# Optimization experiments

Measured on AMD Instinct MI355X. Metric: run time of the kernel, lower is better.

Reference implementation:

```python
import jax, jax.numpy as jnp
import numpy as np

BS, NS, NSTEP = 128, 1024, 8
IN_DIM, HID, MLP = 768, 512, 512
NEG = -100000.0


def setup_inputs() -> dict:
    key = jax.random.key(0)
    ks = jax.random.split(key, 12)
    s_h = 1.0 / np.sqrt(HID)
    s_cat = 1.0 / np.sqrt(HID + IN_DIM)
    s_m = 1.0 / np.sqrt(MLP)
    # gumbel noise implements Categorical sampling as argmax(logits + gumbel)
    u = jax.random.uniform(ks[9], (NSTEP, BS, NS), jnp.float32, 1e-7, 1.0 - 1e-7)
    return {
        "target_emb": jax.random.normal(ks[0], (BS, IN_DIM), jnp.float32),
        "ctx_emb": jax.random.normal(ks[1], (BS, NS, IN_DIM), jnp.float32),
        "target_len": jax.random.randint(ks[2], (BS,), 1, 32),
        "ctx_len": jax.random.randint(ks[3], (BS,), NSTEP, NS + 1),
        "n_step": NSTEP,
        "W_ih": jax.random.normal(ks[4], (4 * HID, IN_DIM), jnp.float32) * s_h,
        "W_hh": jax.random.normal(ks[5], (4 * HID, HID), jnp.float32) * s_h,
        "b_ih": jnp.zeros((4 * HID,), jnp.float32),
        "b_hh": jnp.zeros((4 * HID,), jnp.float32),
        "W1c": jax.random.normal(ks[6], (MLP, IN_DIM), jnp.float32) * s_cat,
        "W1h": jax.random.normal(ks[7], (MLP, HID), jnp.float32) * s_cat,
        "b1": jnp.zeros((MLP,), jnp.float32),
        "w2": jax.random.normal(ks[8], (MLP,), jnp.float32) * s_m,
        "b2": jnp.zeros((), jnp.float32),
        "gumbel": -jnp.log(-jnp.log(u)),
    }


def reference(target_emb, ctx_emb, target_len, ctx_len, n_step,
              W_ih, W_hh, b_ih, b_hh, W1c, W1h, b1, w2, b2, gumbel):
    bs, ns, in_dim = ctx_emb.shape
    hid = W_hh.shape[1]
    # mlp1 split: ctx part is constant across steps (concat([ctx, h]) @ W1^T = ctx@W1c^T + h@W1h^T)
    ctx_part = jnp.einsum('bnd,md->bnm', ctx_emb, W1c) + b1  # [bs, ns, mlp]
    mask0 = jnp.where(jnp.arange(ns)[None, :] >= ctx_len[:, None], NEG, 0.0).astype(jnp.float32)
    h0 = jnp.zeros((bs, hid), jnp.float32)
    c0 = jnp.zeros((bs, hid), jnp.float32)
    lp0 = jnp.zeros((bs,), jnp.float32)
    batch_idx = jnp.arange(bs)

    def step(carry, g):
        h, c, mask, x, lp = carry
        # LSTMCell (torch gate order: i, f, g, o); dropout is identity (eval semantics)
        gates = x @ W_ih.T + b_ih + h @ W_hh.T + b_hh
        i_g, f_g, g_g, o_g = jnp.split(gates, 4, axis=-1)
        c_new = jax.nn.sigmoid(f_g) * c + jax.nn.sigmoid(i_g) * jnp.tanh(g_g)
        h_new = jax.nn.sigmoid(o_g) * jnp.tanh(c_new)
        # attention-style MLP score
        pre = ctx_part + (h_new @ W1h.T)[:, None, :]          # [bs, ns, mlp]
        sc = jnp.tanh(pre) @ w2 + b2 + mask                   # [bs, ns]
        # Categorical(probs=softmax(sc)).sample() via Gumbel-argmax
        out = jnp.argmax(sc + g, axis=-1)                     # [bs]
        lp = lp + jnp.take_along_axis(jax.nn.log_softmax(sc, axis=-1), out[:, None], 1)[:, 0]
        mask = mask.at[batch_idx, out].set(NEG)
        x_new = jnp.take_along_axis(ctx_emb, out[:, None, None], axis=1)[:, 0, :]
        return (h_new, c_new, mask, x_new, lp), out

    (h, c, mask, x, log_probs), outputs = jax.lax.scan(
        step, (h0, c0, mask0, target_emb, lp0), gumbel)
    return outputs, log_probs
```

## Files before the change

kernel.cpp:

```cpp
#include <hip/hip_runtime.h>
#include <hip/hip_bf16.h>

#define BSZ 128
#define NSQ 1024
#define NSTEPC 8
#define IND 768
#define HIDD 512
#define G4D 2048
#define MLPD 512
#define KXD 1280
#define NEGV -100000.0f
#define KSG 16
#define KSH 8
#define MSPLIT 4

typedef __attribute__((ext_vector_type(4))) float f32x4;
typedef __attribute__((ext_vector_type(8))) short short8v;

__device__ __forceinline__ void split2(float4 f0, float4 f1, short8v& hi, short8v& lo) {
  float fv[8] = {f0.x, f0.y, f0.z, f0.w, f1.x, f1.y, f1.z, f1.w};
#pragma unroll
  for (int j = 0; j < 8; ++j) {
    const unsigned ub = __builtin_bit_cast(unsigned, fv[j]);
    const unsigned hb = ub & 0xFFFF0000u;
    const float lf = fv[j] - __builtin_bit_cast(float, hb);
    hi[j] = (short)(hb >> 16);
    lo[j] = (short)(__builtin_bit_cast(unsigned, lf) >> 16);
  }
}

__device__ __forceinline__ float tanh_fast(float x) {
  x = fminf(fmaxf(x, -15.0f), 15.0f);
  float e = __builtin_amdgcn_exp2f(x * 2.8853900817779268f);
  float r = __builtin_amdgcn_rcpf(e + 1.0f);
  return fmaf(-2.0f, r, 1.0f);
}

__global__ __launch_bounds__(256) void k_prep_wfrag(
    const float* __restrict__ W1c,
    unsigned short* __restrict__ wfh, unsigned short* __restrict__ wfl) {
  const int c = blockIdx.x * 256 + threadIdx.x;
  if (c >= 49152) return;
  const int row = c / 96, wc = c - row * 96;
  const int w = row >> 6;
  const int f = (row >> 4) & 3, l15 = row & 15;
  const int t = wc >> 2, l4 = wc & 3;
  const size_t unit = (((size_t)(w * 24 + t) * 4 + f) * 64) + l4 * 16 + l15;
  const float* src = W1c + (size_t)row * IND + wc * 8;
  const float4 f0 = *(const float4*)src, f1 = *(const float4*)(src + 4);
  short8v hi, lo;
  split2(f0, f1, hi, lo);
  *(short8v*)(wfh + unit * 8) = hi;
  *(short8v*)(wfl + unit * 8) = lo;
}

__global__ __launch_bounds__(256) void k_init(
    const float* __restrict__ te, const int* __restrict__ cl,
    float* __restrict__ mask, float* __restrict__ xh,
    float* __restrict__ cst, float* __restrict__ lp) {
  const int b = blockIdx.x, tid = threadIdx.x;
  const int L = cl[b];
  for (int n = tid; n < NSQ; n += 256) mask[(size_t)b*NSQ + n] = (n >= L) ? NEGV : 0.0f;
  for (int d = tid; d < IND; d += 256) xh[(size_t)b*KXD + d] = te[(size_t)b*IND + d];
  for (int j = tid; j < HIDD; j += 256) {
    xh[(size_t)b*KXD + IND + j] = 0.0f;
    cst[(size_t)b*HIDD + j] = 0.0f;
  }
  if (tid == 0) lp[b] = 0.0f;
}

__global__ __launch_bounds__(1024, 1) void k_ctx10(
    const float* __restrict__ ctx,
    const unsigned short* __restrict__ wfh, const unsigned short* __restrict__ wfl,
    const float* __restrict__ bias, const int* __restrict__ clen,
    float* __restrict__ cp) {
  __shared__ __align__(16) unsigned short sCh[2][4096], sCl[2][4096];
  const int strip = blockIdx.x;
  const int b = strip >> 3;
  const int nbase = (strip & 7) << 7;
  if (nbase >= clen[b]) return;
  const int i0 = strip << 7;
  const int tid = threadIdx.x;
  const int lane = tid & 63, wid = tid >> 6;
  const int wm = wid >> 1, wn = wid & 1;
  const int l15 = lane & 15, l4 = lane >> 4;
  const int srow = tid >> 3, sks = tid & 7;
  const int sslot = sks >> 1, shalf = sks & 1;
  const int sswz = (srow >> 1) & 3;
  const float* ssrc = ctx + (size_t)(i0 + srow) * IND + ((sslot ^ sswz) * 8 + shalf * 4);
  const int soff = srow * 32 + sslot * 8 + shalf * 4;
  const size_t wbase = (size_t)(wm * 24) * 2048 + lane * 8;

  auto stage = [&](int t, int buf) {
    const float4 q = *(const float4*)(ssrc + t * 32);
    unsigned h01, h23, l01, l23;
    {
      const float qq[4] = {q.x, q.y, q.z, q.w};
      unsigned hh[4], ll[4];
#pragma unroll
      for (int j = 0; j < 4; ++j) {
        const unsigned ub = __builtin_bit_cast(unsigned, qq[j]);
        const unsigned hb = ub & 0xFFFF0000u;
        const float lf = qq[j] - __builtin_bit_cast(float, hb);
        hh[j] = hb >> 16;
        ll[j] = __builtin_bit_cast(unsigned, lf) >> 16;
      }
      h01 = hh[0] | (hh[1] << 16); h23 = hh[2] | (hh[3] << 16);
      l01 = ll[0] | (ll[1] << 16); l23 = ll[2] | (ll[3] << 16);
    }
    *(uint2*)&sCh[buf][soff] = make_uint2(h01, h23);
    *(uint2*)&sCl[buf][soff] = make_uint2(l01, l23);
  };

  stage(0, 0);

  f32x4 acc[4][4] = {};
  for (int t = 0; t < 24; ++t) {
    __syncthreads();
    const int cur = t & 1;
    short8v wh[4], wl[4];
    const size_t toff = wbase + (size_t)t * 2048;
#pragma unroll
    for (int f = 0; f < 4; ++f) {
      wh[f] = *(const short8v*)(wfh + toff + f * 512);
      wl[f] = *(const short8v*)(wfl + toff + f * 512);
    }
#pragma unroll
    for (int fn = 0; fn < 4; ++fn) {
      const int rc = wn * 64 + fn * 16 + l15;
      const int so = (l4 ^ ((rc >> 1) & 3)) << 3;
      const short8v bhv = *(const short8v*)&sCh[cur][rc * 32 + so];
      const short8v blv = *(const short8v*)&sCl[cur][rc * 32 + so];
      __builtin_amdgcn_s_setprio(1);
#pragma unroll
      for (int fm = 0; fm < 4; ++fm) {
        acc[fm][fn] = __builtin_amdgcn_mfma_f32_16x16x32_bf16(wh[fm], bhv, acc[fm][fn], 0, 0, 0);
        acc[fm][fn] = __builtin_amdgcn_mfma_f32_16x16x32_bf16(wh[fm], blv, acc[fm][fn], 0, 0, 0);
        acc[fm][fn] = __builtin_amdgcn_mfma_f32_16x16x32_bf16(wl[fm], bhv, acc[fm][fn], 0, 0, 0);
      }
      __builtin_amdgcn_s_setprio(0);
    }
    if (t + 1 < 24) stage(t + 1, cur ^ 1);
  }
#pragma unroll
  for (int fm = 0; fm < 4; ++fm) {
#pragma unroll
    for (int r = 0; r < 4; ++r) {
      const int m = wm * 64 + fm * 16 + l4 * 4 + r;
      const float bb = bias[m];
      float* dst = cp + (((size_t)(b * MLPD + m)) << 10) + nbase + wn * 64 + l15;
#pragma unroll
      for (int fn = 0; fn < 4; ++fn)
        dst[fn * 16] = acc[fm][fn][r] + bb;
    }
  }
}

__global__ __launch_bounds__(256) void k_pgemm(
    const float* __restrict__ A, int lda, int acol,
    const float* __restrict__ B0, int ldb0, int kb,
    const float* __restrict__ B1, int ldb1,
    int kTiles, int N, float* __restrict__ P) {
  __shared__ float As[16][128];
  __shared__ float Bs[16][132];
  const int n0 = blockIdx.x * 128;
  const int kc0 = blockIdx.y * kTiles * 16;
  const int tid = threadIdx.x;
  const int tn = tid & 15;
  const int ta = tid >> 4;
  float acc[8][8] = {};
  for (int t = 0; t < kTiles; ++t) {
    const int k0 = kc0 + t * 16;
#pragma unroll
    for (int u = 0; u < 2; ++u) {
      const int v = tid + u * 256;
      const int r = v >> 2, kc = v & 3;
      const float4 a4 = *(const float4*)(A + (size_t)r * lda + acol + k0 + kc * 4);
      As[kc*4+0][r] = a4.x; As[kc*4+1][r] = a4.y; As[kc*4+2][r] = a4.z; As[kc*4+3][r] = a4.w;
      const float* bp = (k0 < kb) ? (B0 + (size_t)(n0 + r) * ldb0 + k0 + kc * 4)
                                  : (B1 + (size_t)(n0 + r) * ldb1 + (k0 - kb) + kc * 4);
      const float4 b4 = *(const float4*)bp;
      Bs[kc*4+0][r] = b4.x; Bs[kc*4+1][r] = b4.y; Bs[kc*4+2][r] = b4.z; Bs[kc*4+3][r] = b4.w;
    }
    __syncthreads();
#pragma unroll
    for (int kk = 0; kk < 16; ++kk) {
      float av[8], bv[8];
#pragma unroll
      for (int q = 0; q < 8; ++q) av[q] = As[kk][ta*8+q];
#pragma unroll
      for (int q = 0; q < 8; ++q) bv[q] = Bs[kk][tn*8+q];
#pragma unroll
      for (int ri = 0; ri < 8; ++ri)
#pragma unroll
        for (int ni = 0; ni < 8; ++ni)
          acc[ri][ni] = fmaf(av[ri], bv[ni], acc[ri][ni]);
    }
    __syncthreads();
  }
#pragma unroll
  for (int ri = 0; ri < 8; ++ri) {
    const int i = ta * 8 + ri;
    float* p = P + ((size_t)blockIdx.y * BSZ + i) * N + n0 + tn * 8;
    *(float4*)(p + 0) = make_float4(acc[ri][0], acc[ri][1], acc[ri][2], acc[ri][3]);
    *(float4*)(p + 4) = make_float4(acc[ri][4], acc[ri][5], acc[ri][6], acc[ri][7]);
  }
}

__global__ __launch_bounds__(512) void k_lstm(
    const float* __restrict__ gp, const float* __restrict__ b_ih,
    const float* __restrict__ b_hh, float* __restrict__ cst, float* __restrict__ xh) {
  const int b = blockIdx.x, j = threadIdx.x;
  float g[4];
#pragma unroll
  for (int q = 0; q < 4; ++q) {
    float s = b_ih[q*HIDD + j] + b_hh[q*HIDD + j];
#pragma unroll
    for (int ks = 0; ks < KSG; ++ks) s += gp[((size_t)ks*BSZ + b)*G4D + q*HIDD + j];
    g[q] = s;
  }
  const float c_old = cst[(size_t)b*HIDD + j];
  const float ig = 1.0f / (1.0f + expf(-g[0]));
  const float fg = 1.0f / (1.0f + expf(-g[1]));
  const float gg = tanhf(g[2]);
  const float og = 1.0f / (1.0f + expf(-g[3]));
  const float cn = fg * c_old + ig * gg;
  const float hn = og * tanhf(cn);
  cst[(size_t)b*HIDD + j] = cn;
  xh[(size_t)b*KXD + IND + j] = hn;
}

__global__ __launch_bounds__(256) void k_scores(
    const float* __restrict__ cp, const float* __restrict__ hpp,
    const float* __restrict__ w2, const int* __restrict__ clen,
    float* __restrict__ psc) {
  const int mh = blockIdx.x;
  const int b = blockIdx.y;
  const int tid = threadIdx.x;
  __shared__ float hs[128], ws[128];
  if (tid < 128) {
    const int m = mh * 128 + tid;
    float s = 0.0f;
#pragma unroll
    for (int ks = 0; ks < KSH; ++ks) s += hpp[((size_t)ks*BSZ + b)*MLPD + m];
    hs[tid] = s;
    ws[tid] = w2[m];
  }
  __syncthreads();
  const int len = clen[b];
  const int n0 = tid * 4;
  if (n0 >= len) return;
  float ax = 0, ay = 0, az = 0, aw = 0;
  const float* base = cp + ((size_t)b * MLPD + mh * 128) * NSQ + n0;
#pragma unroll 4
  for (int mm = 0; mm < 128; ++mm) {
    const float4 c4 = *(const float4*)(base + (size_t)mm * NSQ);
    const float h = hs[mm], w = ws[mm];
    ax = fmaf(tanh_fast(c4.x + h), w, ax);
    ay = fmaf(tanh_fast(c4.y + h), w, ay);
    az = fmaf(tanh_fast(c4.z + h), w, az);
    aw = fmaf(tanh_fast(c4.w + h), w, aw);
  }
  *(float4*)(psc + ((size_t)b * MSPLIT + mh) * NSQ + n0) = make_float4(ax, ay, az, aw);
}

__global__ __launch_bounds__(256) void k_argmax(
    const float* __restrict__ psc, float* __restrict__ mask,
    const float* __restrict__ gum, const float* __restrict__ b2p,
    float* __restrict__ lp, const float* __restrict__ ctx,
    float* __restrict__ xh, float* __restrict__ outv, int step) {
  const int b = blockIdx.x, tid = threadIdx.x;
  __shared__ float rv[256], rs[256], rm[256];
  __shared__ int ri[256];
  __shared__ int sel;
  const float b2 = b2p[0];
  const int n0 = tid * 4;
  const float4 m4 = *(const float4*)(mask + (size_t)b * NSQ + n0);
  float sc[4] = {b2 + m4.x, b2 + m4.y, b2 + m4.z, b2 + m4.w};
#pragma unroll
  for (int mh = 0; mh < MSPLIT; ++mh) {
    const float4 p4 = *(const float4*)(psc + ((size_t)b * MSPLIT + mh) * NSQ + n0);
    sc[0] += p4.x; sc[1] += p4.y; sc[2] += p4.z; sc[3] += p4.w;
  }
  const float4 g4 = *(const float4*)(gum + ((size_t)step * BSZ + b) * NSQ + n0);
  const float gv[4] = {g4.x, g4.y, g4.z, g4.w};
  float bestv = -1e30f, bests = 0.0f, msc = -1e30f;
  int bestn = 0;
#pragma unroll
  for (int q = 0; q < 4; ++q) {
    const float v = sc[q] + gv[q];
    if (v > bestv) { bestv = v; bestn = n0 + q; bests = sc[q]; }
    msc = fmaxf(msc, sc[q]);
  }
  rv[tid] = bestv; ri[tid] = bestn; rs[tid] = bests; rm[tid] = msc;
  __syncthreads();
  for (int o = 128; o > 0; o >>= 1) {
    if (tid < o) {
      if (rv[tid+o] > rv[tid] || (rv[tid+o] == rv[tid] && ri[tid+o] < ri[tid])) {
        rv[tid] = rv[tid+o]; ri[tid] = ri[tid+o]; rs[tid] = rs[tid+o];
      }
      rm[tid] = fmaxf(rm[tid], rm[tid+o]);
    }
    __syncthreads();
  }
  const float M = rm[0];
  __syncthreads();
  float se = 0.0f;
#pragma unroll
  for (int q = 0; q < 4; ++q)
    se += __builtin_amdgcn_exp2f((sc[q] - M) * 1.4426950408889634f);
  rm[tid] = se;
  __syncthreads();
  for (int o = 128; o > 0; o >>= 1) {
    if (tid < o) rm[tid] += rm[tid+o];
    __syncthreads();
  }
  if (tid == 0) {
    const int n = ri[0];
    const float lse = M + logf(rm[0]);
    const float nlp = lp[b] + rs[0] - lse;
    lp[b] = nlp;
    mask[(size_t)b * NSQ + n] = NEGV;
    outv[step * BSZ + b] = (float)n;
    if (step == NSTEPC - 1) outv[NSTEPC * BSZ + b] = nlp;
    sel = n;
  }
  __syncthreads();
  const int n = sel;
  const float4* src = (const float4*)(ctx + ((size_t)b * NSQ + n) * IND);
  float4* dst = (float4*)(xh + (size_t)b * KXD);
  for (int d = tid; d < IND / 4; d += 256) dst[d] = src[d];
}

extern "C" void kernel_launch(void* const* d_in, const int* in_sizes, int n_in,
                              void* d_out, int out_size, void* d_ws, size_t ws_size,
                              hipStream_t stream) {
  const float* target_emb = (const float*)d_in[0];
  const float* ctx_emb   = (const float*)d_in[1];
  const int*   ctx_len   = (const int*)d_in[3];
  const float* W_ih = (const float*)d_in[5];
  const float* W_hh = (const float*)d_in[6];
  const float* b_ih = (const float*)d_in[7];
  const float* b_hh = (const float*)d_in[8];
  const float* W1c  = (const float*)d_in[9];
  const float* W1h  = (const float*)d_in[10];
  const float* b1   = (const float*)d_in[11];
  const float* w2   = (const float*)d_in[12];
  const float* b2   = (const float*)d_in[13];
  const float* gumbel = (const float*)d_in[14];
  float* out = (float*)d_out;

  float* ws = (float*)d_ws;
  size_t off = 0;
  auto alloc = [&](size_t n) { float* p = ws + off; off += (n + 63) & ~(size_t)63; return p; };

  float* cp   = alloc((size_t)BSZ * MLPD * NSQ);
  float* gp   = alloc((size_t)KSG * BSZ * G4D);
  float* hpp  = alloc((size_t)KSH * BSZ * MLPD);
  float* psc  = alloc((size_t)BSZ * MSPLIT * NSQ);
  float* mask = alloc((size_t)BSZ * NSQ);
  float* xh   = alloc((size_t)BSZ * KXD);
  float* cst  = alloc((size_t)BSZ * HIDD);
  float* lp   = alloc(128);
  unsigned short* wfh = (unsigned short*)alloc(196608);
  unsigned short* wfl = (unsigned short*)alloc(196608);

  k_prep_wfrag<<<192, 256, 0, stream>>>(W1c, wfh, wfl);
  k_init<<<BSZ, 256, 0, stream>>>(target_emb, ctx_len, mask, xh, cst, lp);
  k_ctx10<<<1024, 1024, 0, stream>>>(ctx_emb, wfh, wfl, b1, ctx_len, cp);

  for (int t = 0; t < NSTEPC; ++t) {
    k_pgemm<<<dim3(G4D/128, KSG), 256, 0, stream>>>(
        xh, KXD, 0, W_ih, IND, IND, W_hh, HIDD, 5, G4D, gp);
    k_lstm<<<BSZ, 512, 0, stream>>>(gp, b_ih, b_hh, cst, xh);
    k_pgemm<<<dim3(MLPD/128, KSH), 256, 0, stream>>>(
        xh, KXD, IND, W1h, HIDD, 1 << 30, nullptr, 0, 4, MLPD, hpp);
    k_scores<<<dim3(MSPLIT, BSZ), 256, 0, stream>>>(cp, hpp, w2, ctx_len, psc);
    k_argmax<<<BSZ, 256, 0, stream>>>(psc, mask, gumbel, b2, lp, ctx_emb, xh, out, t);
  }
}
```

Measured before the change: 792.8 us.

## Fuse score partial reduction with per-chunk argmax and online log-sum-exp

```diff
diff --git a/kernel.cpp b/kernel.cpp
--- a/kernel.cpp
+++ b/kernel.cpp
@@ -12,7 +12,8 @@
 #define NEGV -100000.0f
 #define KSG 16
 #define KSH 8
-#define MSPLIT 4
+#define NOCT 8
+#define LOG2E 1.4426950408889634f
 
 typedef __attribute__((ext_vector_type(4))) float f32x4;
 typedef __attribute__((ext_vector_type(8))) short short8v;
@@ -230,106 +231,106 @@
   xh[(size_t)b*KXD + IND + j] = hn;
 }
 
-__global__ __launch_bounds__(256) void k_scores(
+__global__ __launch_bounds__(256) void k_nscore(
     const float* __restrict__ cp, const float* __restrict__ hpp,
     const float* __restrict__ w2, const int* __restrict__ clen,
-    float* __restrict__ psc) {
-  const int mh = blockIdx.x;
-  const int b = blockIdx.y;
+    const float* __restrict__ mask, const float* __restrict__ gum,
+    const float* __restrict__ b2p, float* __restrict__ rec, int step) {
+  const int oct = blockIdx.x, b = blockIdx.y;
+  const int len = clen[b];
+  const int n0blk = oct << 7;
+  if (n0blk >= len) return;
+  __shared__ float hs[MLPD], ws[MLPD];
+  __shared__ float2 ps2[4][64];
   const int tid = threadIdx.x;
-  __shared__ float hs[128], ws[128];
-  if (tid < 128) {
-    const int m = mh * 128 + tid;
+  for (int m = tid; m < MLPD; m += 256) {
     float s = 0.0f;
 #pragma unroll
     for (int ks = 0; ks < KSH; ++ks) s += hpp[((size_t)ks*BSZ + b)*MLPD + m];
-    hs[tid] = s;
-    ws[tid] = w2[m];
+    hs[m] = s;
+    ws[m] = w2[m];
   }
   __syncthreads();
-  const int len = clen[b];
-  const int n0 = tid * 4;
-  if (n0 >= len) return;
-  float ax = 0, ay = 0, az = 0, aw = 0;
-  const float* base = cp + ((size_t)b * MLPD + mh * 128) * NSQ + n0;
+  const int mh = tid >> 6, nc = tid & 63;
+  const int n0 = n0blk + nc * 2;
+  float a0 = 0.0f, a1 = 0.0f;
+  {
+    const float* base = cp + (((size_t)(b * MLPD + mh * 128)) << 10) + n0;
+    const float* hp = &hs[mh * 128];
+    const float* wp = &ws[mh * 128];
 #pragma unroll 4
-  for (int mm = 0; mm < 128; ++mm) {
-    const float4 c4 = *(const float4*)(base + (size_t)mm * NSQ);
-    const float h = hs[mm], w = ws[mm];
-    ax = fmaf(tanh_fast(c4.x + h), w, ax);
-    ay = fmaf(tanh_fast(c4.y + h), w, ay);
-    az = fmaf(tanh_fast(c4.z + h), w, az);
-    aw = fmaf(tanh_fast(c4.w + h), w, aw);
-  }
-  *(float4*)(psc + ((size_t)b * MSPLIT + mh) * NSQ + n0) = make_float4(ax, ay, az, aw);
-}
-
-__global__ __launch_bounds__(256) void k_argmax(
-    const float* __restrict__ psc, float* __restrict__ mask,
-    const float* __restrict__ gum, const float* __restrict__ b2p,
-    float* __restrict__ lp, const float* __restrict__ ctx,
-    float* __restrict__ xh, float* __restrict__ outv, int step) {
+    for (int m = 0; m < 128; ++m) {
+      const float2 c2 = *(const float2*)(base + ((size_t)m << 10));
+      const float h = hp[m], w = wp[m];
+      a0 = fmaf(tanh_fast(c2.x + h), w, a0);
+      a1 = fmaf(tanh_fast(c2.y + h), w, a1);
+    }
+  }
+  ps2[mh][nc] = make_float2(a0, a1);
+  __syncthreads();
+  if (tid >= 64) return;
+  const float b2 = b2p[0];
+  const float2 m2 = *(const float2*)(mask + (size_t)b * NSQ + n0);
+  const float2 g2 = *(const float2*)(gum + ((size_t)step * BSZ + b) * NSQ + n0);
+  float sc0 = ps2[0][tid].x + ps2[1][tid].x + ps2[2][tid].x + ps2[3][tid].x + b2 + m2.x;
+  float sc1 = ps2[0][tid].y + ps2[1][tid].y + ps2[2][tid].y + ps2[3][tid].y + b2 + m2.y;
+  const float v0 = sc0 + g2.x, v1 = sc1 + g2.y;
+  float bestv; int bestn; float bests;
+  if (v1 > v0) { bestv = v1; bestn = n0 + 1; bests = sc1; }
+  else         { bestv = v0; bestn = n0;     bests = sc0; }
+  float msc = fmaxf(sc0, sc1);
+#pragma unroll
+  for (int o = 1; o < 64; o <<= 1) msc = fmaxf(msc, __shfl_xor(msc, o));
+  const float M = msc;
+  float se = __builtin_amdgcn_exp2f((sc0 - M) * LOG2E)
+           + __builtin_amdgcn_exp2f((sc1 - M) * LOG2E);
+#pragma unroll
+  for (int o = 1; o < 64; o <<= 1) se += __shfl_xor(se, o);
+#pragma unroll
+  for (int o = 1; o < 64; o <<= 1) {
+    const float ov = __shfl_xor(bestv, o);
+    const int   on = __shfl_xor(bestn, o);
+    const float os = __shfl_xor(bests, o);
+    if (ov > bestv || (ov == bestv && on < bestn)) { bestv = ov; bestn = on; bests = os; }
+  }
+  if (tid == 0) {
+    float* r = rec + (size_t)(b * NOCT + oct) * 8;
+    r[0] = bestv; r[1] = (float)bestn; r[2] = bests; r[3] = M; r[4] = se;
+  }
+}
+
+__global__ __launch_bounds__(192) void k_pick(
+    const float* __restrict__ rec, const int* __restrict__ clen,
+    float* __restrict__ mask, float* __restrict__ lp,
+    const float* __restrict__ ctx, float* __restrict__ xh,
+    float* __restrict__ outv, int step) {
   const int b = blockIdx.x, tid = threadIdx.x;
-  __shared__ float rv[256], rs[256], rm[256];
-  __shared__ int ri[256];
   __shared__ int sel;
-  const float b2 = b2p[0];
-  const int n0 = tid * 4;
-  const float4 m4 = *(const float4*)(mask + (size_t)b * NSQ + n0);
-  float sc[4] = {b2 + m4.x, b2 + m4.y, b2 + m4.z, b2 + m4.w};
-#pragma unroll
-  for (int mh = 0; mh < MSPLIT; ++mh) {
-    const float4 p4 = *(const float4*)(psc + ((size_t)b * MSPLIT + mh) * NSQ + n0);
-    sc[0] += p4.x; sc[1] += p4.y; sc[2] += p4.z; sc[3] += p4.w;
-  }
-  const float4 g4 = *(const float4*)(gum + ((size_t)step * BSZ + b) * NSQ + n0);
-  const float gv[4] = {g4.x, g4.y, g4.z, g4.w};
-  float bestv = -1e30f, bests = 0.0f, msc = -1e30f;
-  int bestn = 0;
-#pragma unroll
-  for (int q = 0; q < 4; ++q) {
-    const float v = sc[q] + gv[q];
-    if (v > bestv) { bestv = v; bestn = n0 + q; bests = sc[q]; }
-    msc = fmaxf(msc, sc[q]);
-  }
-  rv[tid] = bestv; ri[tid] = bestn; rs[tid] = bests; rm[tid] = msc;
-  __syncthreads();
-  for (int o = 128; o > 0; o >>= 1) {
-    if (tid < o) {
-      if (rv[tid+o] > rv[tid] || (rv[tid+o] == rv[tid] && ri[tid+o] < ri[tid])) {
-        rv[tid] = rv[tid+o]; ri[tid] = ri[tid+o]; rs[tid] = rs[tid+o];
-      }
-      rm[tid] = fmaxf(rm[tid], rm[tid+o]);
-    }
-    __syncthreads();
-  }
-  const float M = rm[0];
-  __syncthreads();
-  float se = 0.0f;
-#pragma unroll
-  for (int q = 0; q < 4; ++q)
-    se += __builtin_amdgcn_exp2f((sc[q] - M) * 1.4426950408889634f);
-  rm[tid] = se;
-  __syncthreads();
-  for (int o = 128; o > 0; o >>= 1) {
-    if (tid < o) rm[tid] += rm[tid+o];
-    __syncthreads();
-  }
   if (tid == 0) {
-    const int n = ri[0];
-    const float lse = M + logf(rm[0]);
-    const float nlp = lp[b] + rs[0] - lse;
+    const int nv = (clen[b] + 127) >> 7;
+    const float* r = rec + (size_t)b * NOCT * 8;
+    float bv = r[0]; int bn = (int)r[1]; float bs = r[2];
+    float M = r[3], S = r[4];
+    for (int o = 1; o < nv; ++o) {
+      const float* q = r + o * 8;
+      if (q[0] > bv) { bv = q[0]; bn = (int)q[1]; bs = q[2]; }
+      const float Mq = q[3];
+      const float Mn = fmaxf(M, Mq);
+      S = S * expf(M - Mn) + q[4] * expf(Mq - Mn);
+      M = Mn;
+    }
+    const float nlp = lp[b] + bs - (M + logf(S));
     lp[b] = nlp;
-    mask[(size_t)b * NSQ + n] = NEGV;
-    outv[step * BSZ + b] = (float)n;
+    mask[(size_t)b * NSQ + bn] = NEGV;
+    outv[step * BSZ + b] = (float)bn;
     if (step == NSTEPC - 1) outv[NSTEPC * BSZ + b] = nlp;
-    sel = n;
+    sel = bn;
   }
   __syncthreads();
   const int n = sel;
   const float4* src = (const float4*)(ctx + ((size_t)b * NSQ + n) * IND);
   float4* dst = (float4*)(xh + (size_t)b * KXD);
-  for (int d = tid; d < IND / 4; d += 256) dst[d] = src[d];
+  dst[tid] = src[tid];
 }
 
 extern "C" void kernel_launch(void* const* d_in, const int* in_sizes, int n_in,
@@ -357,7 +358,7 @@
   float* cp   = alloc((size_t)BSZ * MLPD * NSQ);
   float* gp   = alloc((size_t)KSG * BSZ * G4D);
   float* hpp  = alloc((size_t)KSH * BSZ * MLPD);
-  float* psc  = alloc((size_t)BSZ * MSPLIT * NSQ);
+  float* rec  = alloc((size_t)BSZ * NOCT * 8);
   float* mask = alloc((size_t)BSZ * NSQ);
   float* xh   = alloc((size_t)BSZ * KXD);
   float* cst  = alloc((size_t)BSZ * HIDD);
@@ -375,7 +376,8 @@
     k_lstm<<<BSZ, 512, 0, stream>>>(gp, b_ih, b_hh, cst, xh);
     k_pgemm<<<dim3(MLPD/128, KSH), 256, 0, stream>>>(
         xh, KXD, IND, W1h, HIDD, 1 << 30, nullptr, 0, 4, MLPD, hpp);
-    k_scores<<<dim3(MSPLIT, BSZ), 256, 0, stream>>>(cp, hpp, w2, ctx_len, psc);
-    k_argmax<<<BSZ, 256, 0, stream>>>(psc, mask, gumbel, b2, lp, ctx_emb, xh, out, t);
-  }
-}
+    k_nscore<<<dim3(NOCT, BSZ), 256, 0, stream>>>(
+        cp, hpp, w2, ctx_len, mask, gumbel, b2, rec, t);
+    k_pick<<<BSZ, 192, 0, stream>>>(rec, ctx_len, mask, lp, ctx_emb, xh, out, t);
+  }
+}
```

New measurement: 874.7 us. 10.3% more time.
